# Kernel optimization log

Hardware: AMD Instinct MI355X
Metric: run time of the kernel (lower is better)

## Reference

```python
import jax, jax.numpy as jnp
import numpy as np

HEIGHT, WIDTH = 32, 32
NUM_HEADS = 16
FREQUENCY = 10000.0


def _get_thetas(dim, height, width, frequency):
    # dim = head_dim, must be even. Returns (height*width, dim).
    half = dim // 2
    ifreq = 1.0 / (frequency ** (jnp.arange(half, dtype=jnp.float32) / half))
    freqs_h = jnp.arange(height, dtype=jnp.float32)[:, None] * ifreq[None, :]  # (h, half)
    freqs_w = jnp.arange(width, dtype=jnp.float32)[:, None] * ifreq[None, :]   # (w, half)
    theta_h = jnp.broadcast_to(freqs_h[:, None, :], (height, width, half))
    theta_w = jnp.broadcast_to(freqs_w[None, :, :], (height, width, half))
    theta = jnp.concatenate([theta_h, theta_w], axis=-1)  # (h, w, dim)
    return theta.reshape(height * width, dim)


def _add_rope(t, cos, sin):
    # t: (b, h, n, d); cos/sin: (n, d) broadcast over batch and heads
    x1, x2 = jnp.split(t, 2, axis=-1)
    t_rot = jnp.concatenate([-x2, x1], axis=-1)
    return t * cos + t_rot * sin


def setup_inputs() -> dict:
    key = jax.random.key(0)
    k1, k2, k3 = jax.random.split(key, 3)
    b, n, c = 8, HEIGHT * WIDTH, 1024
    tensor = jax.random.normal(k1, (b, n, c), dtype=jnp.float32)
    w_qkv = jax.random.normal(k2, (3 * c, c), dtype=jnp.float32) * (c ** -0.5)
    w_proj = jax.random.normal(k3, (c, c), dtype=jnp.float32) * (c ** -0.5)
    return {"tensor": tensor, "w_qkv": w_qkv, "w_proj": w_proj}


def reference(tensor, w_qkv, w_proj):
    b, n, c = tensor.shape
    hd = c // NUM_HEADS
    # QKV projection, split per-head last dim into q,k,v (matches torch chunk on dim=-1)
    qkv = jnp.einsum('bnc,fc->bnf', tensor, w_qkv)            # (b, n, 3c)
    qkv = qkv.reshape(b, n, NUM_HEADS, 3 * hd).transpose(0, 2, 1, 3)  # (b, H, n, 3*hd)
    q, k, v = jnp.split(qkv, 3, axis=-1)                      # each (b, H, n, hd)
    # 2D RoPE on q, k
    theta = _get_thetas(hd, HEIGHT, WIDTH, FREQUENCY).astype(tensor.dtype)  # (n, hd)
    cos, sin = jnp.cos(theta), jnp.sin(theta)
    q = _add_rope(q, cos, sin)
    k = _add_rope(k, cos, sin)
    # scaled dot product attention
    scale = hd ** -0.5
    scores = jnp.einsum('bhqd,bhkd->bhqk', q, k) * scale
    attn = jax.nn.softmax(scores, axis=-1)
    o = jnp.einsum('bhqk,bhkd->bhqd', attn, v)
    o = o.transpose(0, 2, 1, 3).reshape(b, n, c)
    return jnp.einsum('bnc,oc->bno', o, w_proj)
```

## Files before the change

kernel.cpp:

```cpp
#include <hip/hip_runtime.h>

typedef __attribute__((ext_vector_type(8))) short short8v;
typedef __attribute__((ext_vector_type(4))) float floatx4;
typedef __attribute__((ext_vector_type(4))) unsigned short ushortx4;

__device__ __forceinline__ unsigned short f2bf(float f){
  unsigned int u = __float_as_uint(f);
  u += 0x7fffu + ((u >> 16) & 1u);
  return (unsigned short)(u >> 16);
}

__device__ __forceinline__ void gload_lds16(const void* g, void* l){
  __builtin_amdgcn_global_load_lds((const __attribute__((address_space(1))) void*)g,
                                   (__attribute__((address_space(3))) void*)l, 16, 0, 0);
}

__global__ __launch_bounds__(256) void cvt4(const floatx4* __restrict__ s,
                                            ushortx4* __restrict__ d, int n4){
  int i = blockIdx.x * 256 + threadIdx.x;
  if(i < n4){
    floatx4 v = s[i];
    ushortx4 o;
    #pragma unroll
    for(int j = 0; j < 4; ++j) o[j] = f2bf(v[j]);
    d[i] = o;
  }
}

__global__ __launch_bounds__(256) void cs_init(float2* __restrict__ cs){
  int i = blockIdx.x * 256 + threadIdx.x;
  int p = i >> 6, d = i & 63;
  int y = p >> 5, x = p & 31;
  int dd = d & 31;
  float ifr = powf(10000.0f, -(float)dd * (1.0f / 32.0f));
  float th = (float)(d < 32 ? y : x) * ifr;
  cs[i].x = cosf(th);
  cs[i].y = sinf(th);
}

template<int EPI>
__global__ __launch_bounds__(256) void gemm_bt(
    const unsigned short* __restrict__ A,
    const unsigned short* __restrict__ B,
    int K, int N,
    float* __restrict__ Cf,
    const float2* __restrict__ cs,
    unsigned short* __restrict__ qw,
    unsigned short* __restrict__ kw,
    unsigned short* __restrict__ vtw)
{
  __shared__ unsigned short Al[128 * 32];
  __shared__ unsigned short Bl[128 * 32];
  const int tid = threadIdx.x;
  const int w = tid >> 6, lane = tid & 63;
  const int g = lane >> 4, c0 = lane & 15;
  const int wr = w >> 1, wc = w & 1;
  const size_t m0 = (size_t)blockIdx.y * 128;
  const size_t n0 = (size_t)blockIdx.x * 128;

  floatx4 acc[4][4] = {};

  for(int k0 = 0; k0 < K; k0 += 32){
    #pragma unroll
    for(int q = 0; q < 2; ++q){
      int ci = q * 256 + tid;
      int row = ci >> 2, ko = (ci & 3) << 3;
      gload_lds16(A + (m0 + row) * K + k0 + ko, Al + (size_t)(q * 256 + w * 64) * 8);
      gload_lds16(B + (n0 + row) * K + k0 + ko, Bl + (size_t)(q * 256 + w * 64) * 8);
    }
    __syncthreads();
    short8v am[4], bn[4];
    #pragma unroll
    for(int mf = 0; mf < 4; ++mf)
      am[mf] = *(const short8v*)(Al + (wr * 64 + mf * 16 + c0) * 32 + g * 8);
    #pragma unroll
    for(int nf = 0; nf < 4; ++nf)
      bn[nf] = *(const short8v*)(Bl + (wc * 64 + nf * 16 + c0) * 32 + g * 8);
    #pragma unroll
    for(int mf = 0; mf < 4; ++mf)
      #pragma unroll
      for(int nf = 0; nf < 4; ++nf)
        acc[mf][nf] = __builtin_amdgcn_mfma_f32_16x16x32_bf16(am[mf], bn[nf], acc[mf][nf], 0, 0, 0);
    __syncthreads();
  }

  if(EPI == 0){
    #pragma unroll
    for(int mf = 0; mf < 4; ++mf){
      size_t mrow = m0 + wr * 64 + mf * 16 + g * 4;
      #pragma unroll
      for(int nf = 0; nf < 4; ++nf){
        size_t n = n0 + wc * 64 + nf * 16 + c0;
        #pragma unroll
        for(int r = 0; r < 4; ++r)
          Cf[(mrow + r) * N + n] = acc[mf][nf][r];
      }
    }
  } else {
    int t = (int)(n0 >> 6) + wc;
    int sect = t % 3, hh = t / 3;
    if(sect == 2){
      #pragma unroll
      for(int mf = 0; mf < 4; ++mf){
        size_t m = m0 + wr * 64 + mf * 16 + g * 4;
        int b = (int)(m >> 10); int p = (int)(m & 1023);
        #pragma unroll
        for(int nf = 0; nf < 4; ++nf){
          int d = nf * 16 + c0;
          ushortx4 pk;
          #pragma unroll
          for(int r = 0; r < 4; ++r) pk[r] = f2bf(acc[mf][nf][r]);
          *(ushortx4*)(vtw + ((size_t)(b * 16 + hh) * 64 + d) * 1024 + p) = pk;
        }
      }
    } else {
      unsigned short* dst = (sect == 0) ? qw : kw;
      const float qs = (sect == 0) ? 0.18033688011112042f : 1.0f;
      #pragma unroll
      for(int mf = 0; mf < 4; ++mf){
        #pragma unroll
        for(int r = 0; r < 4; ++r){
          size_t m = m0 + wr * 64 + mf * 16 + g * 4 + r;
          int b = (int)(m >> 10); int p = (int)(m & 1023);
          const float2* csr = cs + (size_t)p * 64;
          unsigned short* orow = dst + ((size_t)(b * 16 + hh) * 1024 + p) * 64;
          #pragma unroll
          for(int nf = 0; nf < 2; ++nf){
            int d = nf * 16 + c0;
            float x1 = acc[mf][nf][r], x2 = acc[mf][nf + 2][r];
            float2 cc1 = csr[d], cc2 = csr[d + 32];
            orow[d]      = f2bf((x1 * cc1.x - x2 * cc1.y) * qs);
            orow[d + 32] = f2bf((x2 * cc2.x + x1 * cc2.y) * qs);
          }
        }
      }
    }
  }
}

__global__ __launch_bounds__(512, 4) void attn_kernel(
    const unsigned short* __restrict__ qw,
    const unsigned short* __restrict__ kw,
    const unsigned short* __restrict__ vtw,
    unsigned short* __restrict__ ow)
{
  __shared__ char smem[65536];
  const int tid = threadIdx.x;
  const int w = tid >> 6, lane = tid & 63;
  const int g = lane >> 4, c0 = lane & 15;
  const int bb = blockIdx.x;
  const int xcd = bb & 7, slot = bb >> 3;
  const int bh = xcd + ((slot >> 2) << 3);
  const int qt = slot & 3;
  const size_t bhoff = (size_t)bh * 1024 * 64;
  const unsigned short* Qb = qw + bhoff;
  const unsigned short* Kb = kw + bhoff;
  const unsigned short* Vb = vtw + bhoff;
  const int q0 = qt * 256 + w * 32;
  char* Pw = smem + 32768 + w * 4096;

  const int srow = tid >> 3;
  const int sjx = ((tid & 7) ^ (srow & 7)) << 3;
  const unsigned short* ksrc = Kb + srow * 64 + sjx;
  const unsigned short* vsrc = Vb + (size_t)srow * 1024 + sjx;
  const int wbase = w * 1024;

  short8v bq[2][2];
  #pragma unroll
  for(int qf = 0; qf < 2; ++qf)
    #pragma unroll
    for(int i = 0; i < 2; ++i)
      bq[qf][i] = *(const short8v*)(Qb + (size_t)(q0 + qf * 16 + c0) * 64 + g * 8 + i * 32);

  floatx4 o[2][4] = {};
  float m_run[2] = {-1e30f, -1e30f};
  float l_part[2] = {0.0f, 0.0f};

  gload_lds16(ksrc, smem + wbase);
  gload_lds16(vsrc, smem + 8192 + wbase);
  __syncthreads();

  int cur = 0;
  for(int kv0 = 0; kv0 < 1024; kv0 += 64){
    char* Ksm = smem + cur * 16384;
    char* Vsm = smem + cur * 16384 + 8192;
    if(kv0 + 64 < 1024){
      char* alt = smem + (cur ^ 1) * 16384;
      gload_lds16(ksrc + (size_t)(kv0 + 64) * 64, alt + wbase);
      gload_lds16(vsrc + kv0 + 64, alt + 8192 + wbase);
    }
    floatx4 st[4][2];
    #pragma unroll
    for(int kf = 0; kf < 4; ++kf){
      const int krow = kf * 16 + c0;
      const char* kr = Ksm + (krow << 7);
      short8v ka0 = *(const short8v*)(kr + (((g    ) ^ (c0 & 7)) << 4));
      short8v ka1 = *(const short8v*)(kr + (((g + 4) ^ (c0 & 7)) << 4));
      #pragma unroll
      for(int qf = 0; qf < 2; ++qf){
        floatx4 z = {};
        z = __builtin_amdgcn_mfma_f32_16x16x32_bf16(ka0, bq[qf][0], z, 0, 0, 0);
        st[kf][qf] = __builtin_amdgcn_mfma_f32_16x16x32_bf16(ka1, bq[qf][1], z, 0, 0, 0);
      }
    }
    float vmax[2];
    #pragma unroll
    for(int qf = 0; qf < 2; ++qf){
      float vm = -1e30f;
      #pragma unroll
      for(int kf = 0; kf < 4; ++kf)
        #pragma unroll
        for(int r = 0; r < 4; ++r) vm = fmaxf(vm, st[kf][qf][r]);
      vm = fmaxf(vm, __shfl_xor(vm, 16));
      vm = fmaxf(vm, __shfl_xor(vm, 32));
      vmax[qf] = vm;
    }
    if(!__all(vmax[0] <= m_run[0] + 8.0f && vmax[1] <= m_run[1] + 8.0f)){
      #pragma unroll
      for(int qf = 0; qf < 2; ++qf){
        float m_new = fmaxf(m_run[qf], vmax[qf]);
        float sc = __builtin_amdgcn_exp2f(m_run[qf] - m_new);
        l_part[qf] *= sc;
        m_run[qf] = m_new;
        float f0 = __shfl(sc, g * 4 + 0);
        float f1 = __shfl(sc, g * 4 + 1);
        float f2 = __shfl(sc, g * 4 + 2);
        float f3 = __shfl(sc, g * 4 + 3);
        #pragma unroll
        for(int nf = 0; nf < 4; ++nf){
          o[qf][nf][0] *= f0; o[qf][nf][1] *= f1; o[qf][nf][2] *= f2; o[qf][nf][3] *= f3;
        }
      }
    }
    #pragma unroll
    for(int qf = 0; qf < 2; ++qf){
      float ps = 0.0f;
      #pragma unroll
      for(int kf = 0; kf < 4; ++kf){
        ushortx4 pk;
        #pragma unroll
        for(int r = 0; r < 4; ++r){
          float e = __builtin_amdgcn_exp2f(st[kf][qf][r] - m_run[qf]);
          ps += e;
          pk[r] = f2bf(e);
        }
        int byo = (qf << 11) + (c0 << 7) + (kf << 5) + (g << 3);
        byo ^= (c0 & 7) << 4;
        *(ushortx4*)(Pw + byo) = pk;
      }
      l_part[qf] += ps;
    }
    short8v pa[2][2];
    #pragma unroll
    for(int mf = 0; mf < 2; ++mf)
      #pragma unroll
      for(int i = 0; i < 2; ++i){
        int byo = (mf << 11) + (c0 << 7) + (i << 6) + (g << 4);
        byo ^= (c0 & 7) << 4;
        pa[mf][i] = *(const short8v*)(Pw + byo);
      }
    #pragma unroll
    for(int nf = 0; nf < 4; ++nf){
      const int vrow = nf * 16 + c0;
      const char* vr = Vsm + (vrow << 7);
      short8v v0 = *(const short8v*)(vr + (((g    ) ^ (c0 & 7)) << 4));
      short8v v1 = *(const short8v*)(vr + (((g + 4) ^ (c0 & 7)) << 4));
      #pragma unroll
      for(int mf = 0; mf < 2; ++mf){
        o[mf][nf] = __builtin_amdgcn_mfma_f32_16x16x32_bf16(pa[mf][0], v0, o[mf][nf], 0, 0, 0);
        o[mf][nf] = __builtin_amdgcn_mfma_f32_16x16x32_bf16(pa[mf][1], v1, o[mf][nf], 0, 0, 0);
      }
    }
    __syncthreads();
    cur ^= 1;
  }

  const int b = bh >> 4, hh = bh & 15;
  #pragma unroll
  for(int mf = 0; mf < 2; ++mf){
    l_part[mf] += __shfl_xor(l_part[mf], 16);
    l_part[mf] += __shfl_xor(l_part[mf], 32);
    float i0 = 1.0f / __shfl(l_part[mf], g * 4 + 0);
    float i1 = 1.0f / __shfl(l_part[mf], g * 4 + 1);
    float i2 = 1.0f / __shfl(l_part[mf], g * 4 + 2);
    float i3 = 1.0f / __shfl(l_part[mf], g * 4 + 3);
    #pragma unroll
    for(int nf = 0; nf < 4; ++nf){
      o[mf][nf][0] *= i0; o[mf][nf][1] *= i1; o[mf][nf][2] *= i2; o[mf][nf][3] *= i3;
      #pragma unroll
      for(int r = 0; r < 4; ++r){
        size_t row = (size_t)b * 1024 + q0 + mf * 16 + g * 4 + r;
        ow[row * 1024 + hh * 64 + nf * 16 + c0] = f2bf(o[mf][nf][r]);
      }
    }
  }
}


extern "C" void kernel_launch(void* const* d_in, const int* in_sizes, int n_in,
                              void* d_out, int out_size, void* d_ws, size_t ws_size,
                              hipStream_t stream){
  const float* tensor = (const float*)d_in[0];
  const float* w_qkv  = (const float*)d_in[1];
  const float* w_proj = (const float*)d_in[2];
  char* ws = (char*)d_ws;
  unsigned short* bfT  = (unsigned short*)(ws);
  unsigned short* bfWq = (unsigned short*)(ws + 16777216);
  unsigned short* bfWp = (unsigned short*)(ws + 23068672);
  float2*         cs   = (float2*)        (ws + 25165824);
  unsigned short* qw   = (unsigned short*)(ws + 25690112);
  unsigned short* kw   = (unsigned short*)(ws + 42467328);
  unsigned short* vtw  = (unsigned short*)(ws + 59244544);
  unsigned short* owp  = (unsigned short*)(ws + 76021760);

  cvt4<<<8192, 256, 0, stream>>>((const floatx4*)tensor, (ushortx4*)bfT, 2097152);
  cvt4<<<3072, 256, 0, stream>>>((const floatx4*)w_qkv,  (ushortx4*)bfWq, 786432);
  cvt4<<<1024, 256, 0, stream>>>((const floatx4*)w_proj, (ushortx4*)bfWp, 262144);
  cs_init<<<256, 256, 0, stream>>>(cs);

  gemm_bt<1><<<dim3(24, 64), 256, 0, stream>>>(bfT, bfWq, 1024, 3072,
                                               nullptr, cs, qw, kw, vtw);
  attn_kernel<<<512, 512, 0, stream>>>(qw, kw, vtw, owp);
  gemm_bt<0><<<dim3(8, 64), 256, 0, stream>>>(owp, bfWp, 1024, 1024,
                                              (float*)d_out, nullptr, nullptr, nullptr, nullptr);
}
```

Before: 185.3 us.

## Replace GEMM with 256x256-tile double-buffered pipelined 8-wave kernel

Replaces the simple 128x128, single-buffered bf16 MFMA GEMM with a 256x256-tile, 512-thread kernel. It double-buffers 64-wide K tiles in 128KB of LDS and interleaves async global-to-LDS loads with MFMA phases using barriers, setprio and manual vmcnt waits. It also adds an XOR swizzle to avoid LDS bank conflicts and remaps block IDs so neighbouring workgroups share tiles in the same XCD. The goal is to hide memory latency and raise MFMA utilisation for the QKV and output projections. The trade-offs are fewer blocks (384 and 128), so less parallelism on the smaller GEMM, and a more fragile hand-written schedule.

After: 175.1 us. -5.5%, faster.

```diff
diff --git a/kernel.cpp b/kernel.cpp
--- a/kernel.cpp
+++ b/kernel.cpp
@@ -39,70 +39,152 @@
 }
 
 template<int EPI>
-__global__ __launch_bounds__(256) void gemm_bt(
+__global__ __launch_bounds__(512, 2) void gemm8(
     const unsigned short* __restrict__ A,
     const unsigned short* __restrict__ B,
-    int K, int N,
+    int K, int N, int NXB,
     float* __restrict__ Cf,
     const float2* __restrict__ cs,
     unsigned short* __restrict__ qw,
     unsigned short* __restrict__ kw,
     unsigned short* __restrict__ vtw)
 {
-  __shared__ unsigned short Al[128 * 32];
-  __shared__ unsigned short Bl[128 * 32];
+  __shared__ char lds[131072];
   const int tid = threadIdx.x;
   const int w = tid >> 6, lane = tid & 63;
   const int g = lane >> 4, c0 = lane & 15;
-  const int wr = w >> 1, wc = w & 1;
-  const size_t m0 = (size_t)blockIdx.y * 128;
-  const size_t n0 = (size_t)blockIdx.x * 128;
-
-  floatx4 acc[4][4] = {};
-
-  for(int k0 = 0; k0 < K; k0 += 32){
-    #pragma unroll
-    for(int q = 0; q < 2; ++q){
-      int ci = q * 256 + tid;
-      int row = ci >> 2, ko = (ci & 3) << 3;
-      gload_lds16(A + (m0 + row) * K + k0 + ko, Al + (size_t)(q * 256 + w * 64) * 8);
-      gload_lds16(B + (n0 + row) * K + k0 + ko, Bl + (size_t)(q * 256 + w * 64) * 8);
-    }
-    __syncthreads();
+  const int wm = w >> 2, wn = w & 3;
+  const int NT = K >> 6;
+
+  const int per = gridDim.x >> 3;
+  const int wg = (blockIdx.x & 7) * per + (blockIdx.x >> 3);
+  const int by = wg / NXB, bx = wg % NXB;
+  const size_t m0 = (size_t)by * 256;
+  const size_t n0 = (size_t)bx * 256;
+
+  const int row0 = tid >> 2;
+  const int xch = (tid & 3) ^ ((tid >> 3) & 3);
+  const unsigned short* sA0 = A + (m0 + row0) * K + xch * 8;
+  const unsigned short* sA1 = A + (m0 + row0 + 128) * K + xch * 8;
+  const unsigned short* sB0 = B + (n0 + row0) * K + xch * 8;
+  const unsigned short* sB1 = B + (n0 + row0 + 128) * K + xch * 8;
+  char* const Ald = lds;
+  char* const Bld = lds + 65536;
+  const int wb = w * 1024;
+
+  auto stA = [&](int t, int buf, int kh){
+    char* d = Ald + buf * 32768 + kh * 16384 + wb;
+    gload_lds16(sA0 + t * 64 + kh * 32, d);
+    gload_lds16(sA1 + t * 64 + kh * 32, d + 8192);
+  };
+  auto stB = [&](int t, int buf, int kh){
+    char* d = Bld + buf * 32768 + kh * 16384 + wb;
+    gload_lds16(sB0 + t * 64 + kh * 32, d);
+    gload_lds16(sB1 + t * 64 + kh * 32, d + 8192);
+  };
+
+  const int archy = (g ^ ((c0 >> 1) & 3)) << 4;
+  auto rdA = [&](int buf, int kh, int mf) -> short8v {
+    return *(const short8v*)(Ald + buf * 32768 + kh * 16384 +
+                             (wm * 128 + mf * 16 + c0) * 64 + archy);
+  };
+  auto rdB = [&](int buf, int kh, int nf) -> short8v {
+    return *(const short8v*)(Bld + buf * 32768 + kh * 16384 +
+                             (wn * 64 + nf * 16 + c0) * 64 + archy);
+  };
+
+  floatx4 acc[8][4] = {};
+
+#define BARX() do{ __builtin_amdgcn_s_barrier(); __builtin_amdgcn_sched_barrier(0); }while(0)
+
+  auto tile4 = [&](int t, int buf){
+    const int ob = buf ^ 1;
+    const int tn1 = (t + 1 < NT) ? t + 1 : NT - 1;
+    const int tn2 = (t + 2 < NT) ? t + 2 : NT - 1;
     short8v am[4], bn[4];
     #pragma unroll
-    for(int mf = 0; mf < 4; ++mf)
-      am[mf] = *(const short8v*)(Al + (wr * 64 + mf * 16 + c0) * 32 + g * 8);
-    #pragma unroll
-    for(int nf = 0; nf < 4; ++nf)
-      bn[nf] = *(const short8v*)(Bl + (wc * 64 + nf * 16 + c0) * 32 + g * 8);
+    for(int nf = 0; nf < 4; ++nf) bn[nf] = rdB(buf, 0, nf);
+    #pragma unroll
+    for(int mf = 0; mf < 4; ++mf) am[mf] = rdA(buf, 0, mf);
+    stA(tn1, ob, 1); stB(tn1, ob, 1);
+    BARX();
+    __builtin_amdgcn_s_setprio(1);
     #pragma unroll
     for(int mf = 0; mf < 4; ++mf)
       #pragma unroll
       for(int nf = 0; nf < 4; ++nf)
         acc[mf][nf] = __builtin_amdgcn_mfma_f32_16x16x32_bf16(am[mf], bn[nf], acc[mf][nf], 0, 0, 0);
-    __syncthreads();
-  }
+    __builtin_amdgcn_s_setprio(0);
+    BARX();
+    #pragma unroll
+    for(int mf = 0; mf < 4; ++mf) am[mf] = rdA(buf, 0, 4 + mf);
+    BARX();
+    __builtin_amdgcn_s_setprio(1);
+    #pragma unroll
+    for(int mf = 0; mf < 4; ++mf)
+      #pragma unroll
+      for(int nf = 0; nf < 4; ++nf)
+        acc[4 + mf][nf] = __builtin_amdgcn_mfma_f32_16x16x32_bf16(am[mf], bn[nf], acc[4 + mf][nf], 0, 0, 0);
+    __builtin_amdgcn_s_setprio(0);
+    BARX();
+    #pragma unroll
+    for(int nf = 0; nf < 4; ++nf) bn[nf] = rdB(buf, 1, nf);
+    #pragma unroll
+    for(int mf = 0; mf < 4; ++mf) am[mf] = rdA(buf, 1, mf);
+    stA(tn2, buf, 0);
+    BARX();
+    __builtin_amdgcn_s_setprio(1);
+    #pragma unroll
+    for(int mf = 0; mf < 4; ++mf)
+      #pragma unroll
+      for(int nf = 0; nf < 4; ++nf)
+        acc[mf][nf] = __builtin_amdgcn_mfma_f32_16x16x32_bf16(am[mf], bn[nf], acc[mf][nf], 0, 0, 0);
+    __builtin_amdgcn_s_setprio(0);
+    BARX();
+    #pragma unroll
+    for(int mf = 0; mf < 4; ++mf) am[mf] = rdA(buf, 1, 4 + mf);
+    stB(tn2, buf, 0);
+    BARX();
+    __builtin_amdgcn_s_setprio(1);
+    #pragma unroll
+    for(int mf = 0; mf < 4; ++mf)
+      #pragma unroll
+      for(int nf = 0; nf < 4; ++nf)
+        acc[4 + mf][nf] = __builtin_amdgcn_mfma_f32_16x16x32_bf16(am[mf], bn[nf], acc[4 + mf][nf], 0, 0, 0);
+    __builtin_amdgcn_s_setprio(0);
+    asm volatile("s_waitcnt vmcnt(4)" ::: "memory");
+    BARX();
+  };
+
+  stA(0, 0, 0); stB(0, 0, 0);
+  stA(0, 0, 1); stB(0, 0, 1);
+  stA(1, 1, 0); stB(1, 1, 0);
+  asm volatile("s_waitcnt vmcnt(4)" ::: "memory");
+  BARX();
+
+  for(int t = 0; t < NT; t += 2){ tile4(t, 0); tile4(t + 1, 1); }
+  __syncthreads();
+#undef BARX
 
   if(EPI == 0){
     #pragma unroll
-    for(int mf = 0; mf < 4; ++mf){
-      size_t mrow = m0 + wr * 64 + mf * 16 + g * 4;
+    for(int mf = 0; mf < 8; ++mf){
+      size_t mrow = m0 + wm * 128 + mf * 16 + g * 4;
       #pragma unroll
       for(int nf = 0; nf < 4; ++nf){
-        size_t n = n0 + wc * 64 + nf * 16 + c0;
+        size_t n = n0 + wn * 64 + nf * 16 + c0;
         #pragma unroll
         for(int r = 0; r < 4; ++r)
           Cf[(mrow + r) * N + n] = acc[mf][nf][r];
       }
     }
   } else {
-    int t = (int)(n0 >> 6) + wc;
+    int t = (int)(n0 >> 6) + wn;
     int sect = t % 3, hh = t / 3;
     if(sect == 2){
       #pragma unroll
-      for(int mf = 0; mf < 4; ++mf){
-        size_t m = m0 + wr * 64 + mf * 16 + g * 4;
+      for(int mf = 0; mf < 8; ++mf){
+        size_t m = m0 + wm * 128 + mf * 16 + g * 4;
         int b = (int)(m >> 10); int p = (int)(m & 1023);
         #pragma unroll
         for(int nf = 0; nf < 4; ++nf){
@@ -117,10 +199,10 @@
       unsigned short* dst = (sect == 0) ? qw : kw;
       const float qs = (sect == 0) ? 0.18033688011112042f : 1.0f;
       #pragma unroll
-      for(int mf = 0; mf < 4; ++mf){
+      for(int mf = 0; mf < 8; ++mf){
         #pragma unroll
         for(int r = 0; r < 4; ++r){
-          size_t m = m0 + wr * 64 + mf * 16 + g * 4 + r;
+          size_t m = m0 + wm * 128 + mf * 16 + g * 4 + r;
           int b = (int)(m >> 10); int p = (int)(m & 1023);
           const float2* csr = cs + (size_t)p * 64;
           unsigned short* orow = dst + ((size_t)(b * 16 + hh) * 1024 + p) * 64;
@@ -318,9 +400,9 @@
   cvt4<<<1024, 256, 0, stream>>>((const floatx4*)w_proj, (ushortx4*)bfWp, 262144);
   cs_init<<<256, 256, 0, stream>>>(cs);
 
-  gemm_bt<1><<<dim3(24, 64), 256, 0, stream>>>(bfT, bfWq, 1024, 3072,
-                                               nullptr, cs, qw, kw, vtw);
+  gemm8<1><<<384, 512, 0, stream>>>(bfT, bfWq, 1024, 3072, 12,
+                                    nullptr, cs, qw, kw, vtw);
   attn_kernel<<<512, 512, 0, stream>>>(qw, kw, vtw, owp);
-  gemm_bt<0><<<dim3(8, 64), 256, 0, stream>>>(owp, bfWp, 1024, 1024,
-                                              (float*)d_out, nullptr, nullptr, nullptr, nullptr);
-}
+  gemm8<0><<<128, 512, 0, stream>>>(owp, bfWp, 1024, 1024, 4,
+                                    (float*)d_out, nullptr, nullptr, nullptr, nullptr);
+}
```
